# Performance work log

Hardware: AMD Instinct MI355X
Metric: run time of the kernel (lower is better)

## Reference

```python
import jax, jax.numpy as jnp
import numpy as np

B, N, CQ, H, CH = 1, 256, 128, 4, 32  # batch, n_res, c_q(=c_k=c_v), heads, per-head dim


def setup_inputs() -> dict:
    key = jax.random.key(0)
    ks = jax.random.split(key, 12)
    s = 0.02
    q_x = jax.random.normal(ks[0], (B, N, N, CQ), jnp.float32)
    kv_x = jax.random.normal(ks[1], (B, N, N, CQ), jnp.float32)
    # mask bias: 0 where kept, -1e9 where masked (additive mask)
    keep = jax.random.uniform(ks[2], (B, N, 1, 1, N)) < 0.9
    mask_bias = jnp.where(keep, 0.0, -1e9).astype(jnp.float32)
    triangle_bias = jax.random.normal(ks[3], (B, 1, H, N, N), jnp.float32)
    # projection weights, stored per-head as [H, CH, C_in]
    wq = jax.random.normal(ks[4], (H, CH, CQ), jnp.float32) * s
    wk = jax.random.normal(ks[5], (H, CH, CQ), jnp.float32) * s
    wv = jax.random.normal(ks[6], (H, CH, CQ), jnp.float32) * s
    wg = jax.random.normal(ks[7], (H, CH, CQ), jnp.float32) * s
    bg = jax.random.normal(ks[8], (H, CH), jnp.float32) * s + 1.0  # gating bias init 1
    wo = jax.random.normal(ks[9], (CQ, H * CH), jnp.float32) * s
    bo = jnp.zeros((CQ,), jnp.float32)
    return {"q_x": q_x, "kv_x": kv_x, "mask_bias": mask_bias,
            "triangle_bias": triangle_bias, "wq": wq, "wk": wk, "wv": wv,
            "wg": wg, "bg": bg, "wo": wo, "bo": bo}


def reference(q_x, kv_x, mask_bias, triangle_bias, wq, wk, wv, wg, bg, wo, bo):
    scale = 1.0 / np.sqrt(CH).astype(np.float32)
    # project + split heads: [B,N,Q,C] x [H,D,C] -> [B,N,H,Q,D]
    q = jnp.einsum('bnqc,hdc->bnhqd', q_x, wq) * scale
    k = jnp.einsum('bnkc,hdc->bnhkd', kv_x, wk)
    v = jnp.einsum('bnkc,hdc->bnhkd', kv_x, wv)
    # scores + additive biases (mask_bias broadcasts over h,q; triangle over n)
    a = jnp.einsum('bnhqd,bnhkd->bnhqk', q, k) + mask_bias + triangle_bias
    a = jax.nn.softmax(a, axis=-1)
    o = jnp.einsum('bnhqk,bnhkd->bnhqd', a, v)
    o = jnp.swapaxes(o, -2, -3)  # [B,N,Q,H,D]
    # gating
    g = jax.nn.sigmoid(jnp.einsum('bnqc,hdc->bnqhd', q_x, wg) + bg)
    o = o * g
    o = o.reshape(o.shape[:-2] + (H * CH,))  # [B,N,Q,H*D]
    return jnp.einsum('bnqe,ce->bnqc', o, wo) + bo
```

## Files before the change

kernel.cpp:

```cpp
#include <hip/hip_runtime.h>

#define NRES 256
#define CIN  128
#define NH   4
#define DH   32

typedef __attribute__((ext_vector_type(4))) float f32x4;
typedef __attribute__((ext_vector_type(8))) short bf16x8;
typedef unsigned short u16;

#define U_WQG 0
#define U_WKV 32768
#define U_WWO 65536
#define U_QB  131072
#define U_KB  (U_QB + 8388608)
#define U_VT  (U_KB + 8388608)
#define U_GB  (U_VT + 8388608)
#define WS_NEED ((size_t)(U_GB + 8388608) * 2)

__device__ __forceinline__ unsigned pkbf(float a, float b) {
    unsigned ua = __builtin_bit_cast(unsigned, a);
    unsigned ub = __builtin_bit_cast(unsigned, b);
    ua += 0x7fffu + ((ua >> 16) & 1u);
    ub += 0x7fffu + ((ub >> 16) & 1u);
    return __builtin_amdgcn_perm(ub, ua, 0x07060302);
}
__device__ __forceinline__ u16 f2bfu(float f) {
    unsigned u = __builtin_bit_cast(unsigned, f);
    return (u16)((u + 0x7fffu + ((u >> 16) & 1u)) >> 16);
}
__device__ __forceinline__ float bf2f(u16 v) {
    unsigned u = ((unsigned)v) << 16;
    return __builtin_bit_cast(float, u);
}
union bfr { unsigned u[4]; bf16x8 v; };
__device__ __forceinline__ bf16x8 ldcvt8(const float* __restrict__ p) {
    f32x4 a = *(const f32x4*)p; f32x4 b = *(const f32x4*)(p + 4);
    bfr r;
    r.u[0] = pkbf(a[0], a[1]); r.u[1] = pkbf(a[2], a[3]);
    r.u[2] = pkbf(b[0], b[1]); r.u[3] = pkbf(b[2], b[3]);
    return r.v;
}
__device__ __forceinline__ bf16x8 ldcvt8s(const float* __restrict__ p, float sc) {
    f32x4 a = *(const f32x4*)p; f32x4 b = *(const f32x4*)(p + 4);
    bfr r;
    r.u[0] = pkbf(a[0] * sc, a[1] * sc); r.u[1] = pkbf(a[2] * sc, a[3] * sc);
    r.u[2] = pkbf(b[0] * sc, b[1] * sc); r.u[3] = pkbf(b[2] * sc, b[3] * sc);
    return r.v;
}
#define MFMA(a, b, c) __builtin_amdgcn_mfma_f32_16x16x32_bf16((a), (b), (c), 0, 0, 0)

__global__ void wconv(const float* __restrict__ wq, const float* __restrict__ wk,
                      const float* __restrict__ wv, const float* __restrict__ wg,
                      const float* __restrict__ wo, u16* __restrict__ ws)
{
    const int i0 = (blockIdx.x * 256 + threadIdx.x) * 8;
    const float qsc = 0.17677669529663687f;
    const float* src; u16* dst; float sc = 1.f;
    if (i0 < 32768) {
        const int e = i0 >> 7, c = i0 & 127;
        src = (e < 128 ? wq + e * CIN : wg + (e - 128) * CIN) + c;
        if (e < 128) sc = qsc;
        dst = ws + U_WQG + i0;
    } else if (i0 < 65536) {
        const int j = i0 - 32768, e = j >> 7, c = j & 127;
        src = (e < 128 ? wk + e * CIN : wv + (e - 128) * CIN) + c;
        dst = ws + U_WKV + j;
    } else {
        const int j = i0 - 65536;
        src = wo + j; dst = ws + U_WWO + j;
    }
    *(bf16x8*)dst = ldcvt8s(src, sc);
}

__global__ __launch_bounds__(256, 4) void proj(
    const float* __restrict__ q_x, const float* __restrict__ kv_x,
    const float* __restrict__ bg, u16* __restrict__ ws)
{
    const int t = threadIdx.x, lane = t & 63, w = t >> 6;
    const int mrow = lane & 15, grp = lane >> 4;
    const int koff = grp * 8, rbase = grp * 4;
    const int R0 = blockIdx.x * 64;
    const int e0 = w * 64;
    const int ysel = blockIdx.y;
    const float* __restrict__ src = ysel ? kv_x : q_x;
    const u16* __restrict__ W = ws + (ysel ? U_WKV : U_WQG);
    const bool vpath = (ysel == 1) && (w >= 2);

    const f32x4 zf = {0.f, 0.f, 0.f, 0.f};
    f32x4 acc[4][4];
    #pragma unroll
    for (int mt = 0; mt < 4; ++mt)
        #pragma unroll
        for (int nt = 0; nt < 4; ++nt) acc[mt][nt] = zf;

    if (!vpath) {
        #pragma unroll 1
        for (int ct = 0; ct < 4; ++ct) {
            const int c0 = ct * 32 + koff;
            const bf16x8 bw0 = *(const bf16x8*)(W + (e0 +  0 + mrow) * CIN + c0);
            const bf16x8 bw1 = *(const bf16x8*)(W + (e0 + 16 + mrow) * CIN + c0);
            const bf16x8 bw2 = *(const bf16x8*)(W + (e0 + 32 + mrow) * CIN + c0);
            const bf16x8 bw3 = *(const bf16x8*)(W + (e0 + 48 + mrow) * CIN + c0);
            #pragma unroll
            for (int mt = 0; mt < 4; ++mt) {
                const bf16x8 aX = ldcvt8(src + (size_t)(R0 + mt * 16 + mrow) * CIN + c0);
                acc[mt][0] = MFMA(bw0, aX, acc[mt][0]);
                acc[mt][1] = MFMA(bw1, aX, acc[mt][1]);
                acc[mt][2] = MFMA(bw2, aX, acc[mt][2]);
                acc[mt][3] = MFMA(bw3, aX, acc[mt][3]);
            }
        }
    } else {
        #pragma unroll 1
        for (int ct = 0; ct < 4; ++ct) {
            const int c0 = ct * 32 + koff;
            const bf16x8 bw0 = *(const bf16x8*)(W + (e0 +  0 + mrow) * CIN + c0);
            const bf16x8 bw1 = *(const bf16x8*)(W + (e0 + 16 + mrow) * CIN + c0);
            const bf16x8 bw2 = *(const bf16x8*)(W + (e0 + 32 + mrow) * CIN + c0);
            const bf16x8 bw3 = *(const bf16x8*)(W + (e0 + 48 + mrow) * CIN + c0);
            #pragma unroll
            for (int mt = 0; mt < 4; ++mt) {
                const bf16x8 aX = ldcvt8(src + (size_t)(R0 + mt * 16 + mrow) * CIN + c0);
                acc[mt][0] = MFMA(aX, bw0, acc[mt][0]);
                acc[mt][1] = MFMA(aX, bw1, acc[mt][1]);
                acc[mt][2] = MFMA(aX, bw2, acc[mt][2]);
                acc[mt][3] = MFMA(aX, bw3, acc[mt][3]);
            }
        }
    }

    if (!ysel) {
        if (w < 2) {
            #pragma unroll
            for (int mt = 0; mt < 4; ++mt) {
                const size_t row = (size_t)(R0 + mt * 16 + mrow);
                #pragma unroll
                for (int nt = 0; nt < 4; ++nt) {
                    uint2 v;
                    v.x = pkbf(acc[mt][nt][0], acc[mt][nt][1]);
                    v.y = pkbf(acc[mt][nt][2], acc[mt][nt][3]);
                    *(uint2*)&ws[U_QB + row * CIN + e0 + nt * 16 + rbase] = v;
                }
            }
        } else {
            #pragma unroll
            for (int mt = 0; mt < 4; ++mt) {
                const size_t row = (size_t)(R0 + mt * 16 + mrow);
                #pragma unroll
                for (int nt = 0; nt < 4; ++nt) {
                    const int eb = (e0 - 128) + nt * 16 + rbase;
                    const f32x4 bgv = *(const f32x4*)(bg + eb);
                    float g[4];
                    #pragma unroll
                    for (int r = 0; r < 4; ++r)
                        g[r] = 1.f / (1.f + __expf(-(acc[mt][nt][r] + bgv[r])));
                    uint2 v;
                    v.x = pkbf(g[0], g[1]);
                    v.y = pkbf(g[2], g[3]);
                    *(uint2*)&ws[U_GB + row * CIN + eb] = v;
                }
            }
        }
    } else {
        if (w < 2) {
            #pragma unroll
            for (int mt = 0; mt < 4; ++mt) {
                const size_t row = (size_t)(R0 + mt * 16 + mrow);
                #pragma unroll
                for (int nt = 0; nt < 4; ++nt) {
                    uint2 v;
                    v.x = pkbf(acc[mt][nt][0], acc[mt][nt][1]);
                    v.y = pkbf(acc[mt][nt][2], acc[mt][nt][3]);
                    *(uint2*)&ws[U_KB + row * CIN + e0 + nt * 16 + rbase] = v;
                }
            }
        } else {
            const int n = R0 >> 8;
            #pragma unroll
            for (int mt = 0; mt < 4; ++mt) {
                const int k0 = (R0 & 255) + mt * 16 + rbase;
                #pragma unroll
                for (int nt = 0; nt < 4; ++nt) {
                    const int d = (e0 - 128) + nt * 16 + mrow;
                    uint2 v;
                    v.x = pkbf(acc[mt][nt][0], acc[mt][nt][1]);
                    v.y = pkbf(acc[mt][nt][2], acc[mt][nt][3]);
                    *(uint2*)&ws[U_VT + ((size_t)n * 128 + d) * 256 + k0] = v;
                }
            }
        }
    }
}

#define PST 40
__global__ __launch_bounds__(256, 4) void flash(
    const u16* __restrict__ ws, const float* __restrict__ mask_bias,
    const float* __restrict__ tri_bias, float* __restrict__ o_out)
{
    const int h = blockIdx.x, n = blockIdx.y;
    const int t = threadIdx.x, lane = t & 63, w = t >> 6;
    const int mrow = lane & 15, grp = lane >> 4;
    const int koff = grp * 8, rbase = grp * 4;
    const int q0 = w * 64;

    __shared__ u16 Pt[4 * 64 * PST];
    __shared__ float msk[NRES];

    if (t < 64) *(float4*)&msk[t * 4] = *(const float4*)(mask_bias + n * NRES + t * 4);

    const u16* __restrict__ Qb = ws + U_QB + (size_t)n * NRES * CIN;
    const u16* __restrict__ Kb = ws + U_KB + (size_t)n * NRES * CIN;
    const u16* __restrict__ Vt = ws + U_VT + (size_t)n * 128 * 256;
    const u16* __restrict__ Gb = ws + U_GB + (size_t)n * NRES * CIN;
    const float* __restrict__ trih = tri_bias + (size_t)h * NRES * NRES;

    bf16x8 aq[4];
    #pragma unroll
    for (int qt = 0; qt < 4; ++qt)
        aq[qt] = *(const bf16x8*)(Qb + (size_t)(q0 + qt * 16 + mrow) * CIN + h * DH + koff);
    __syncthreads();

    const f32x4 zf = {0.f, 0.f, 0.f, 0.f};
    f32x4 oa[4][2], ls4[4];
    #pragma unroll
    for (int qt = 0; qt < 4; ++qt) { oa[qt][0] = zf; oa[qt][1] = zf; ls4[qt] = zf; }

    u16* __restrict__ pw = &Pt[w * 64 * PST];

    for (int kt = 0; kt < 8; ++kt) {
        const int kb = kt * 32;
        bf16x8 bk0 = *(const bf16x8*)(Kb + (size_t)(kb + mrow) * CIN + h * DH + koff);
        bf16x8 bk1 = *(const bf16x8*)(Kb + (size_t)(kb + 16 + mrow) * CIN + h * DH + koff);
        bf16x8 bv0 = *(const bf16x8*)(Vt + (size_t)(h * DH + mrow) * NRES + kb + koff);
        bf16x8 bv1 = *(const bf16x8*)(Vt + (size_t)(h * DH + 16 + mrow) * NRES + kb + koff);
        const float mb0 = msk[kb + mrow] - 8.f;
        const float mb1 = msk[kb + 16 + mrow] - 8.f;

        #pragma unroll
        for (int h2 = 0; h2 < 2; ++h2) {
            float tr0[2][4], tr1[2][4];
            #pragma unroll
            for (int j = 0; j < 2; ++j) {
                const int qt = h2 * 2 + j;
                const float* __restrict__ trow =
                    trih + (q0 + qt * 16 + rbase) * NRES + kb + mrow;
                #pragma unroll
                for (int r = 0; r < 4; ++r) {
                    tr0[j][r] = trow[r * NRES];
                    tr1[j][r] = trow[r * NRES + 16];
                }
            }
            #pragma unroll
            for (int j = 0; j < 2; ++j) {
                const int qt = h2 * 2 + j;
                f32x4 s0 = MFMA(aq[qt], bk0, zf);
                f32x4 s1 = MFMA(aq[qt], bk1, zf);
                #pragma unroll
                for (int r = 0; r < 4; ++r) {
                    s0[r] = __expf(s0[r] + tr0[j][r] + mb0);
                    s1[r] = __expf(s1[r] + tr1[j][r] + mb1);
                }
                ls4[qt] += s0 + s1;
                #pragma unroll
                for (int r = 0; r < 4; ++r) {
                    pw[(qt * 16 + rbase + r) * PST + mrow]      = f2bfu(s0[r]);
                    pw[(qt * 16 + rbase + r) * PST + 16 + mrow] = f2bfu(s1[r]);
                }
            }
        }
        asm volatile("s_waitcnt lgkmcnt(0)" ::: "memory");
        #pragma unroll
        for (int qt = 0; qt < 4; ++qt) {
            bf16x8 pa = *(const bf16x8*)&pw[(qt * 16 + mrow) * PST + koff];
            oa[qt][0] = MFMA(pa, bv0, oa[qt][0]);
            oa[qt][1] = MFMA(pa, bv1, oa[qt][1]);
        }
    }

    float* __restrict__ orow = o_out + (size_t)n * NRES * CIN + h * DH;
    #pragma unroll
    for (int qt = 0; qt < 4; ++qt) {
        f32x4 lv = ls4[qt];
        #pragma unroll
        for (int xm = 1; xm < 16; xm <<= 1) {
            lv[0] += __shfl_xor(lv[0], xm, 64);
            lv[1] += __shfl_xor(lv[1], xm, 64);
            lv[2] += __shfl_xor(lv[2], xm, 64);
            lv[3] += __shfl_xor(lv[3], xm, 64);
        }
        #pragma unroll
        for (int r = 0; r < 4; ++r) {
            const float inv = 1.f / lv[r];
            const int q = q0 + qt * 16 + rbase + r;
            const float g0 = bf2f(Gb[(size_t)q * CIN + h * DH + mrow]);
            const float g1 = bf2f(Gb[(size_t)q * CIN + h * DH + 16 + mrow]);
            orow[q * CIN + mrow]      = oa[qt][0][r] * inv * g0;
            orow[q * CIN + 16 + mrow] = oa[qt][1][r] * inv * g1;
        }
    }
}

__global__ __launch_bounds__(256, 4) void gout(
    const u16* __restrict__ ws, const float* __restrict__ bo, float* io)
{
    const int t = threadIdx.x, lane = t & 63, w = t >> 6;
    const int mrow = lane & 15, grp = lane >> 4;
    const int koff = grp * 8, rbase = grp * 4;
    const int r0 = blockIdx.x * 128 + w * 32;
    const u16* __restrict__ Wo = ws + U_WWO;

    const f32x4 zf = {0.f, 0.f, 0.f, 0.f};
    f32x4 acc[2][8];
    #pragma unroll
    for (int at = 0; at < 2; ++at)
        #pragma unroll
        for (int nt = 0; nt < 8; ++nt) acc[at][nt] = zf;

    #pragma unroll
    for (int ks = 0; ks < 4; ++ks) {
        const int e0 = ks * 32 + koff;
        bf16x8 a0 = ldcvt8(io + (size_t)(r0 + mrow) * CIN + e0);
        bf16x8 a1 = ldcvt8(io + (size_t)(r0 + 16 + mrow) * CIN + e0);
        #pragma unroll
        for (int nt = 0; nt < 8; ++nt) {
            bf16x8 bw = *(const bf16x8*)(Wo + (nt * 16 + mrow) * CIN + e0);
            acc[0][nt] = MFMA(a0, bw, acc[0][nt]);
            acc[1][nt] = MFMA(a1, bw, acc[1][nt]);
        }
    }

    #pragma unroll
    for (int nt = 0; nt < 8; ++nt) {
        const float bc = bo[nt * 16 + mrow];
        #pragma unroll
        for (int at = 0; at < 2; ++at)
            #pragma unroll
            for (int r = 0; r < 4; ++r)
                io[(size_t)(r0 + at * 16 + rbase + r) * CIN + nt * 16 + mrow] =
                    acc[at][nt][r] + bc;
    }
}

#define KST 32
#define VST 264
#define GST 136

__global__ __launch_bounds__(256, 3) void attn_fb(
    const float* __restrict__ q_x, const float* __restrict__ kv_x,
    const float* __restrict__ mask_bias, const float* __restrict__ tri_bias,
    const float* __restrict__ wq, const float* __restrict__ wk,
    const float* __restrict__ wv, float* __restrict__ o_out)
{
    const int h = blockIdx.x, n = blockIdx.y;
    const int t = threadIdx.x;
    const int lane = t & 63, w = t >> 6;
    const int mrow = lane & 15;
    const int grp  = lane >> 4;
    const int koff = grp * 8;
    const int rbase = grp * 4;
    const int q0 = w * 64;

    __shared__ u16 Ks[NRES * KST];
    __shared__ u16 Vt[DH * VST];
    __shared__ u16 Ptb[4 * 32 * PST];
    __shared__ float msk[NRES];

    if (t < 64) *(float4*)&msk[t * 4] = *(const float4*)(mask_bias + n * NRES + t * 4);

    const float* __restrict__ qxn = q_x  + (size_t)n * NRES * CIN;
    const float* __restrict__ kxn = kv_x + (size_t)n * NRES * CIN;
    const float* __restrict__ wqh = wq + h * DH * CIN;
    const float* __restrict__ wkh = wk + h * DH * CIN;
    const float* __restrict__ wvh = wv + h * DH * CIN;

    f32x4 aq_[4][2], ak_[4][2], av_[4][2];
    const f32x4 zf = {0.f, 0.f, 0.f, 0.f};
    #pragma unroll
    for (int qt = 0; qt < 4; ++qt)
        #pragma unroll
        for (int dt = 0; dt < 2; ++dt) { aq_[qt][dt] = zf; ak_[qt][dt] = zf; av_[qt][dt] = zf; }

    const float qsc = 0.17677669529663687f;
    #pragma unroll
    for (int ct = 0; ct < 4; ++ct) {
        const int c0 = ct * 32 + koff;
        bf16x8 bq0 = ldcvt8s(wqh + mrow * CIN + c0, qsc);
        bf16x8 bq1 = ldcvt8s(wqh + (16 + mrow) * CIN + c0, qsc);
        bf16x8 bk0 = ldcvt8(wkh + mrow * CIN + c0);
        bf16x8 bk1 = ldcvt8(wkh + (16 + mrow) * CIN + c0);
        bf16x8 bv0 = ldcvt8(wvh + mrow * CIN + c0);
        bf16x8 bv1 = ldcvt8(wvh + (16 + mrow) * CIN + c0);
        #pragma unroll
        for (int qt = 0; qt < 4; ++qt) {
            bf16x8 aX = ldcvt8(qxn + (q0 + qt * 16 + mrow) * CIN + c0);
            aq_[qt][0] = MFMA(aX, bq0, aq_[qt][0]);
            aq_[qt][1] = MFMA(aX, bq1, aq_[qt][1]);
            bf16x8 aK = ldcvt8(kxn + (q0 + qt * 16 + mrow) * CIN + c0);
            ak_[qt][0] = MFMA(aK, bk0, ak_[qt][0]);
            ak_[qt][1] = MFMA(aK, bk1, ak_[qt][1]);
            av_[qt][0] = MFMA(aK, bv0, av_[qt][0]);
            av_[qt][1] = MFMA(aK, bv1, av_[qt][1]);
        }
    }

    #pragma unroll
    for (int qt = 0; qt < 4; ++qt)
        #pragma unroll
        for (int dt = 0; dt < 2; ++dt)
            #pragma unroll
            for (int r = 0; r < 4; ++r) {
                const int row = q0 + qt * 16 + rbase + r;
                const int d = dt * 16 + mrow;
                Ks[row * KST + d] = f2bfu(ak_[qt][dt][r]);
                Vt[d * VST + row] = f2bfu(av_[qt][dt][r]);
            }

    u16* __restrict__ pw = &Ptb[w * 32 * PST];
    bf16x8 aq[4];
    #pragma unroll
    for (int h2 = 0; h2 < 2; ++h2) {
        #pragma unroll
        for (int j = 0; j < 2; ++j) {
            const int qt = h2 * 2 + j;
            #pragma unroll
            for (int dt = 0; dt < 2; ++dt)
                #pragma unroll
                for (int r = 0; r < 4; ++r)
                    pw[(j * 16 + rbase + r) * PST + dt * 16 + mrow] = f2bfu(aq_[qt][dt][r]);
        }
        asm volatile("s_waitcnt lgkmcnt(0)" ::: "memory");
        #pragma unroll
        for (int j = 0; j < 2; ++j)
            aq[h2 * 2 + j] = *(const bf16x8*)&pw[(j * 16 + mrow) * PST + koff];
        asm volatile("s_waitcnt lgkmcnt(0)" ::: "memory");
    }
    __syncthreads();

    f32x4 oa[4][2], ls4[4];
    #pragma unroll
    for (int qt = 0; qt < 4; ++qt) { oa[qt][0] = zf; oa[qt][1] = zf; ls4[qt] = zf; }

    const float* __restrict__ trih = tri_bias + (size_t)h * NRES * NRES;

    for (int kt = 0; kt < 8; ++kt) {
        const int kb = kt * 32;
        bf16x8 bk0 = *(const bf16x8*)&Ks[(kb + mrow) * KST + koff];
        bf16x8 bk1 = *(const bf16x8*)&Ks[(kb + 16 + mrow) * KST + koff];
        bf16x8 bv0 = *(const bf16x8*)&Vt[mrow * VST + kb + koff];
        bf16x8 bv1 = *(const bf16x8*)&Vt[(16 + mrow) * VST + kb + koff];
        const float mb0 = msk[kb + mrow] - 8.f;
        const float mb1 = msk[kb + 16 + mrow] - 8.f;

        #pragma unroll
        for (int h2 = 0; h2 < 2; ++h2) {
            float tr0[2][4], tr1[2][4];
            #pragma unroll
            for (int j = 0; j < 2; ++j) {
                const int qt = h2 * 2 + j;
                const float* __restrict__ trow =
                    trih + (q0 + qt * 16 + rbase) * NRES + kb + mrow;
                #pragma unroll
                for (int r = 0; r < 4; ++r) {
                    tr0[j][r] = trow[r * NRES];
                    tr1[j][r] = trow[r * NRES + 16];
                }
            }
            #pragma unroll
            for (int j = 0; j < 2; ++j) {
                const int qt = h2 * 2 + j;
                f32x4 s0 = MFMA(aq[qt], bk0, zf);
                f32x4 s1 = MFMA(aq[qt], bk1, zf);
                #pragma unroll
                for (int r = 0; r < 4; ++r) {
                    s0[r] = __expf(s0[r] + tr0[j][r] + mb0);
                    s1[r] = __expf(s1[r] + tr1[j][r] + mb1);
                }
                ls4[qt] += s0 + s1;
                #pragma unroll
                for (int r = 0; r < 4; ++r) {
                    pw[(j * 16 + rbase + r) * PST + mrow]      = f2bfu(s0[r]);
                    pw[(j * 16 + rbase + r) * PST + 16 + mrow] = f2bfu(s1[r]);
                }
            }
            asm volatile("s_waitcnt lgkmcnt(0)" ::: "memory");
            #pragma unroll
            for (int j = 0; j < 2; ++j) {
                const int qt = h2 * 2 + j;
                bf16x8 pa = *(const bf16x8*)&pw[(j * 16 + mrow) * PST + koff];
                oa[qt][0] = MFMA(pa, bv0, oa[qt][0]);
                oa[qt][1] = MFMA(pa, bv1, oa[qt][1]);
            }
        }
    }

    float* __restrict__ orow = o_out + (size_t)n * NRES * CIN + h * DH;
    #pragma unroll
    for (int qt = 0; qt < 4; ++qt) {
        f32x4 lv = ls4[qt];
        #pragma unroll
        for (int xm = 1; xm < 16; xm <<= 1) {
            lv[0] += __shfl_xor(lv[0], xm, 64);
            lv[1] += __shfl_xor(lv[1], xm, 64);
            lv[2] += __shfl_xor(lv[2], xm, 64);
            lv[3] += __shfl_xor(lv[3], xm, 64);
        }
        #pragma unroll
        for (int r = 0; r < 4; ++r) {
            const float inv = 1.f / lv[r];
            const int q = q0 + qt * 16 + rbase + r;
            orow[q * CIN + mrow]      = oa[qt][0][r] * inv;
            orow[q * CIN + 16 + mrow] = oa[qt][1][r] * inv;
        }
    }
}

__global__ __launch_bounds__(256, 4) void gate_fb(
    const float* __restrict__ q_x, const float* __restrict__ wg,
    const float* __restrict__ bg, const float* __restrict__ wo,
    const float* __restrict__ bo, float* io)
{
    const int t = threadIdx.x;
    const int lane = t & 63, w = t >> 6;
    const int mrow = lane & 15, grp = lane >> 4;
    const int koff = grp * 8, rbase = grp * 4;
    const int r0 = blockIdx.x * 128 + w * 32;

    __shared__ u16 Gt[4 * 32 * GST];
    u16* __restrict__ gw = &Gt[w * 32 * GST];

    const f32x4 zf = {0.f, 0.f, 0.f, 0.f};
    f32x4 acc[2][8];
    #pragma unroll
    for (int at = 0; at < 2; ++at)
        #pragma unroll
        for (int nt = 0; nt < 8; ++nt) acc[at][nt] = zf;

    #pragma unroll
    for (int ks = 0; ks < 4; ++ks) {
        const int c0 = ks * 32 + koff;
        bf16x8 ax0 = ldcvt8(q_x + (size_t)(r0 + mrow) * CIN + c0);
        bf16x8 ax1 = ldcvt8(q_x + (size_t)(r0 + 16 + mrow) * CIN + c0);
        #pragma unroll
        for (int nt = 0; nt < 8; ++nt) {
            bf16x8 bw = ldcvt8(wg + (nt * 16 + mrow) * CIN + c0);
            acc[0][nt] = MFMA(ax0, bw, acc[0][nt]);
            acc[1][nt] = MFMA(ax1, bw, acc[1][nt]);
        }
    }

    #pragma unroll
    for (int nt = 0; nt < 8; ++nt) {
        const float bge = bg[nt * 16 + mrow];
        #pragma unroll
        for (int at = 0; at < 2; ++at)
            #pragma unroll
            for (int r = 0; r < 4; ++r) {
                const int qg = r0 + at * 16 + rbase + r;
                const float ov = io[(size_t)qg * CIN + nt * 16 + mrow];
                const float g = 1.f / (1.f + __expf(-(acc[at][nt][r] + bge)));
                gw[(at * 16 + rbase + r) * GST + nt * 16 + mrow] = f2bfu(ov * g);
            }
    }
    asm volatile("s_waitcnt lgkmcnt(0)" ::: "memory");

    f32x4 acc2[2][8];
    #pragma unroll
    for (int at = 0; at < 2; ++at)
        #pragma unroll
        for (int nt = 0; nt < 8; ++nt) acc2[at][nt] = zf;

    #pragma unroll
    for (int ks = 0; ks < 4; ++ks) {
        const int e0 = ks * 32 + koff;
        bf16x8 ag0 = *(const bf16x8*)&gw[mrow * GST + e0];
        bf16x8 ag1 = *(const bf16x8*)&gw[(16 + mrow) * GST + e0];
        #pragma unroll
        for (int nt = 0; nt < 8; ++nt) {
            bf16x8 bw = ldcvt8(wo + (nt * 16 + mrow) * CIN + e0);
            acc2[0][nt] = MFMA(ag0, bw, acc2[0][nt]);
            acc2[1][nt] = MFMA(ag1, bw, acc2[1][nt]);
        }
    }

    #pragma unroll
    for (int nt = 0; nt < 8; ++nt) {
        const float boc = bo[nt * 16 + mrow];
        #pragma unroll
        for (int at = 0; at < 2; ++at)
            #pragma unroll
            for (int r = 0; r < 4; ++r)
                io[(size_t)(r0 + at * 16 + rbase + r) * CIN + nt * 16 + mrow] =
                    acc2[at][nt][r] + boc;
    }
}

extern "C" void kernel_launch(void* const* d_in, const int* in_sizes, int n_in,
                              void* d_out, int out_size, void* d_ws, size_t ws_size,
                              hipStream_t stream) {
    const float* q_x  = (const float*)d_in[0];
    const float* kv_x = (const float*)d_in[1];
    const float* mask = (const float*)d_in[2];
    const float* tri  = (const float*)d_in[3];
    const float* wq   = (const float*)d_in[4];
    const float* wk   = (const float*)d_in[5];
    const float* wv   = (const float*)d_in[6];
    const float* wg   = (const float*)d_in[7];
    const float* bg   = (const float*)d_in[8];
    const float* wo   = (const float*)d_in[9];
    const float* bo   = (const float*)d_in[10];
    float* out = (float*)d_out;

    if (ws_size >= WS_NEED) {
        u16* ws16 = (u16*)d_ws;
        wconv<<<40, 256, 0, stream>>>(wq, wk, wv, wg, wo, ws16);
        proj<<<dim3(1024, 2), 256, 0, stream>>>(q_x, kv_x, bg, ws16);
        flash<<<dim3(NH, NRES), 256, 0, stream>>>(ws16, mask, tri, out);
        gout<<<512, 256, 0, stream>>>(ws16, bo, out);
    } else {
        attn_fb<<<dim3(NH, NRES), 256, 0, stream>>>(q_x, kv_x, mask, tri, wq, wk, wv, out);
        gate_fb<<<(NRES * NRES) / 128, 256, 0, stream>>>(q_x, wg, bg, wo, bo, out);
    }
}
```

Measured before the change: 232.7 us.

## Fuse projection, attention and output GEMM into one per-row kernel

Replaces the separate proj, flash and gout launches with a single kernel that runs one block per residue row n. Each block first computes the Q/G/K/V projections for its 256 rows, then loops over the four heads doing the attention, and writes the gated output as bf16 into the Q buffer in place. It then runs the output projection from that buffer and adds the bias. This removes two kernel launches and the fp32 round trip of the intermediate attention output through global memory. In exchange the grid drops to 256 blocks of 4 waves each, which is far less parallelism and latency hiding than the earlier grids, and the per-head work inside a block runs serially.

```diff
diff --git a/kernel.cpp b/kernel.cpp
--- a/kernel.cpp
+++ b/kernel.cpp
@@ -73,272 +73,270 @@
     *(bf16x8*)dst = ldcvt8s(src, sc);
 }
 
-__global__ __launch_bounds__(256, 4) void proj(
+#define PST 40
+__global__ __launch_bounds__(256) void fused(
     const float* __restrict__ q_x, const float* __restrict__ kv_x,
-    const float* __restrict__ bg, u16* __restrict__ ws)
+    const float* __restrict__ bg, const float* __restrict__ mask_bias,
+    const float* __restrict__ tri_bias, const float* __restrict__ bo,
+    u16* __restrict__ ws, float* __restrict__ out)
 {
+    const int n = blockIdx.x;
     const int t = threadIdx.x, lane = t & 63, w = t >> 6;
     const int mrow = lane & 15, grp = lane >> 4;
     const int koff = grp * 8, rbase = grp * 4;
-    const int R0 = blockIdx.x * 64;
-    const int e0 = w * 64;
-    const int ysel = blockIdx.y;
-    const float* __restrict__ src = ysel ? kv_x : q_x;
-    const u16* __restrict__ W = ws + (ysel ? U_WKV : U_WQG);
-    const bool vpath = (ysel == 1) && (w >= 2);
-
-    const f32x4 zf = {0.f, 0.f, 0.f, 0.f};
-    f32x4 acc[4][4];
-    #pragma unroll
-    for (int mt = 0; mt < 4; ++mt)
-        #pragma unroll
-        for (int nt = 0; nt < 4; ++nt) acc[mt][nt] = zf;
-
-    if (!vpath) {
-        #pragma unroll 1
-        for (int ct = 0; ct < 4; ++ct) {
-            const int c0 = ct * 32 + koff;
-            const bf16x8 bw0 = *(const bf16x8*)(W + (e0 +  0 + mrow) * CIN + c0);
-            const bf16x8 bw1 = *(const bf16x8*)(W + (e0 + 16 + mrow) * CIN + c0);
-            const bf16x8 bw2 = *(const bf16x8*)(W + (e0 + 32 + mrow) * CIN + c0);
-            const bf16x8 bw3 = *(const bf16x8*)(W + (e0 + 48 + mrow) * CIN + c0);
-            #pragma unroll
-            for (int mt = 0; mt < 4; ++mt) {
-                const bf16x8 aX = ldcvt8(src + (size_t)(R0 + mt * 16 + mrow) * CIN + c0);
-                acc[mt][0] = MFMA(bw0, aX, acc[mt][0]);
-                acc[mt][1] = MFMA(bw1, aX, acc[mt][1]);
-                acc[mt][2] = MFMA(bw2, aX, acc[mt][2]);
-                acc[mt][3] = MFMA(bw3, aX, acc[mt][3]);
-            }
-        }
-    } else {
-        #pragma unroll 1
-        for (int ct = 0; ct < 4; ++ct) {
-            const int c0 = ct * 32 + koff;
-            const bf16x8 bw0 = *(const bf16x8*)(W + (e0 +  0 + mrow) * CIN + c0);
-            const bf16x8 bw1 = *(const bf16x8*)(W + (e0 + 16 + mrow) * CIN + c0);
-            const bf16x8 bw2 = *(const bf16x8*)(W + (e0 + 32 + mrow) * CIN + c0);
-            const bf16x8 bw3 = *(const bf16x8*)(W + (e0 + 48 + mrow) * CIN + c0);
-            #pragma unroll
-            for (int mt = 0; mt < 4; ++mt) {
-                const bf16x8 aX = ldcvt8(src + (size_t)(R0 + mt * 16 + mrow) * CIN + c0);
-                acc[mt][0] = MFMA(aX, bw0, acc[mt][0]);
-                acc[mt][1] = MFMA(aX, bw1, acc[mt][1]);
-                acc[mt][2] = MFMA(aX, bw2, acc[mt][2]);
-                acc[mt][3] = MFMA(aX, bw3, acc[mt][3]);
-            }
-        }
-    }
-
-    if (!ysel) {
-        if (w < 2) {
-            #pragma unroll
-            for (int mt = 0; mt < 4; ++mt) {
-                const size_t row = (size_t)(R0 + mt * 16 + mrow);
-                #pragma unroll
-                for (int nt = 0; nt < 4; ++nt) {
-                    uint2 v;
-                    v.x = pkbf(acc[mt][nt][0], acc[mt][nt][1]);
-                    v.y = pkbf(acc[mt][nt][2], acc[mt][nt][3]);
-                    *(uint2*)&ws[U_QB + row * CIN + e0 + nt * 16 + rbase] = v;
-                }
-            }
-        } else {
-            #pragma unroll
-            for (int mt = 0; mt < 4; ++mt) {
-                const size_t row = (size_t)(R0 + mt * 16 + mrow);
-                #pragma unroll
-                for (int nt = 0; nt < 4; ++nt) {
-                    const int eb = (e0 - 128) + nt * 16 + rbase;
-                    const f32x4 bgv = *(const f32x4*)(bg + eb);
-                    float g[4];
-                    #pragma unroll
-                    for (int r = 0; r < 4; ++r)
-                        g[r] = 1.f / (1.f + __expf(-(acc[mt][nt][r] + bgv[r])));
-                    uint2 v;
-                    v.x = pkbf(g[0], g[1]);
-                    v.y = pkbf(g[2], g[3]);
-                    *(uint2*)&ws[U_GB + row * CIN + eb] = v;
-                }
-            }
-        }
-    } else {
-        if (w < 2) {
-            #pragma unroll
-            for (int mt = 0; mt < 4; ++mt) {
-                const size_t row = (size_t)(R0 + mt * 16 + mrow);
-                #pragma unroll
-                for (int nt = 0; nt < 4; ++nt) {
-                    uint2 v;
-                    v.x = pkbf(acc[mt][nt][0], acc[mt][nt][1]);
-                    v.y = pkbf(acc[mt][nt][2], acc[mt][nt][3]);
-                    *(uint2*)&ws[U_KB + row * CIN + e0 + nt * 16 + rbase] = v;
-                }
-            }
-        } else {
-            const int n = R0 >> 8;
-            #pragma unroll
-            for (int mt = 0; mt < 4; ++mt) {
-                const int k0 = (R0 & 255) + mt * 16 + rbase;
-                #pragma unroll
-                for (int nt = 0; nt < 4; ++nt) {
-                    const int d = (e0 - 128) + nt * 16 + mrow;
-                    uint2 v;
-                    v.x = pkbf(acc[mt][nt][0], acc[mt][nt][1]);
-                    v.y = pkbf(acc[mt][nt][2], acc[mt][nt][3]);
-                    *(uint2*)&ws[U_VT + ((size_t)n * 128 + d) * 256 + k0] = v;
-                }
-            }
-        }
-    }
-}
-
-#define PST 40
-__global__ __launch_bounds__(256, 4) void flash(
-    const u16* __restrict__ ws, const float* __restrict__ mask_bias,
-    const float* __restrict__ tri_bias, float* __restrict__ o_out)
-{
-    const int h = blockIdx.x, n = blockIdx.y;
-    const int t = threadIdx.x, lane = t & 63, w = t >> 6;
-    const int mrow = lane & 15, grp = lane >> 4;
-    const int koff = grp * 8, rbase = grp * 4;
-    const int q0 = w * 64;
 
     __shared__ u16 Pt[4 * 64 * PST];
     __shared__ float msk[NRES];
 
     if (t < 64) *(float4*)&msk[t * 4] = *(const float4*)(mask_bias + n * NRES + t * 4);
 
-    const u16* __restrict__ Qb = ws + U_QB + (size_t)n * NRES * CIN;
+    #pragma unroll 1
+    for (int u = 0; u < 8; ++u) {
+        const int tid  = u * 4 + w;
+        const int ysel = tid & 1;
+        const int rb   = (tid >> 1) & 3;
+        const int e0   = ((tid >> 3) & 3) * 64;
+        const int R0   = n * 256 + rb * 64;
+        const float* __restrict__ src = ysel ? kv_x : q_x;
+        const u16* __restrict__ W = ws + (ysel ? U_WKV : U_WQG);
+        const bool vpath = ysel && (e0 >= 128);
+
+        const f32x4 zf = {0.f, 0.f, 0.f, 0.f};
+        f32x4 acc[4][4];
+        #pragma unroll
+        for (int mt = 0; mt < 4; ++mt)
+            #pragma unroll
+            for (int nt = 0; nt < 4; ++nt) acc[mt][nt] = zf;
+
+        if (!vpath) {
+            #pragma unroll 2
+            for (int ct = 0; ct < 4; ++ct) {
+                const int c0 = ct * 32 + koff;
+                const bf16x8 bw0 = *(const bf16x8*)(W + (e0 +  0 + mrow) * CIN + c0);
+                const bf16x8 bw1 = *(const bf16x8*)(W + (e0 + 16 + mrow) * CIN + c0);
+                const bf16x8 bw2 = *(const bf16x8*)(W + (e0 + 32 + mrow) * CIN + c0);
+                const bf16x8 bw3 = *(const bf16x8*)(W + (e0 + 48 + mrow) * CIN + c0);
+                #pragma unroll
+                for (int mt = 0; mt < 4; ++mt) {
+                    const bf16x8 aX = ldcvt8(src + (size_t)(R0 + mt * 16 + mrow) * CIN + c0);
+                    acc[mt][0] = MFMA(bw0, aX, acc[mt][0]);
+                    acc[mt][1] = MFMA(bw1, aX, acc[mt][1]);
+                    acc[mt][2] = MFMA(bw2, aX, acc[mt][2]);
+                    acc[mt][3] = MFMA(bw3, aX, acc[mt][3]);
+                }
+            }
+        } else {
+            #pragma unroll 2
+            for (int ct = 0; ct < 4; ++ct) {
+                const int c0 = ct * 32 + koff;
+                const bf16x8 bw0 = *(const bf16x8*)(W + (e0 +  0 + mrow) * CIN + c0);
+                const bf16x8 bw1 = *(const bf16x8*)(W + (e0 + 16 + mrow) * CIN + c0);
+                const bf16x8 bw2 = *(const bf16x8*)(W + (e0 + 32 + mrow) * CIN + c0);
+                const bf16x8 bw3 = *(const bf16x8*)(W + (e0 + 48 + mrow) * CIN + c0);
+                #pragma unroll
+                for (int mt = 0; mt < 4; ++mt) {
+                    const bf16x8 aX = ldcvt8(src + (size_t)(R0 + mt * 16 + mrow) * CIN + c0);
+                    acc[mt][0] = MFMA(aX, bw0, acc[mt][0]);
+                    acc[mt][1] = MFMA(aX, bw1, acc[mt][1]);
+                    acc[mt][2] = MFMA(aX, bw2, acc[mt][2]);
+                    acc[mt][3] = MFMA(aX, bw3, acc[mt][3]);
+                }
+            }
+        }
+
+        if (!ysel) {
+            if (e0 < 128) {
+                #pragma unroll
+                for (int mt = 0; mt < 4; ++mt) {
+                    const size_t row = (size_t)(R0 + mt * 16 + mrow);
+                    #pragma unroll
+                    for (int nt = 0; nt < 4; ++nt) {
+                        uint2 v;
+                        v.x = pkbf(acc[mt][nt][0], acc[mt][nt][1]);
+                        v.y = pkbf(acc[mt][nt][2], acc[mt][nt][3]);
+                        *(uint2*)&ws[U_QB + row * CIN + e0 + nt * 16 + rbase] = v;
+                    }
+                }
+            } else {
+                #pragma unroll
+                for (int mt = 0; mt < 4; ++mt) {
+                    const size_t row = (size_t)(R0 + mt * 16 + mrow);
+                    #pragma unroll
+                    for (int nt = 0; nt < 4; ++nt) {
+                        const int eb = (e0 - 128) + nt * 16 + rbase;
+                        const f32x4 bgv = *(const f32x4*)(bg + eb);
+                        float g[4];
+                        #pragma unroll
+                        for (int r = 0; r < 4; ++r)
+                            g[r] = 1.f / (1.f + __expf(-(acc[mt][nt][r] + bgv[r])));
+                        uint2 v;
+                        v.x = pkbf(g[0], g[1]);
+                        v.y = pkbf(g[2], g[3]);
+                        *(uint2*)&ws[U_GB + row * CIN + eb] = v;
+                    }
+                }
+            }
+        } else {
+            if (e0 < 128) {
+                #pragma unroll
+                for (int mt = 0; mt < 4; ++mt) {
+                    const size_t row = (size_t)(R0 + mt * 16 + mrow);
+                    #pragma unroll
+                    for (int nt = 0; nt < 4; ++nt) {
+                        uint2 v;
+                        v.x = pkbf(acc[mt][nt][0], acc[mt][nt][1]);
+                        v.y = pkbf(acc[mt][nt][2], acc[mt][nt][3]);
+                        *(uint2*)&ws[U_KB + row * CIN + e0 + nt * 16 + rbase] = v;
+                    }
+                }
+            } else {
+                #pragma unroll
+                for (int mt = 0; mt < 4; ++mt) {
+                    const int k0 = rb * 64 + mt * 16 + rbase;
+                    #pragma unroll
+                    for (int nt = 0; nt < 4; ++nt) {
+                        const int d = (e0 - 128) + nt * 16 + mrow;
+                        uint2 v;
+                        v.x = pkbf(acc[mt][nt][0], acc[mt][nt][1]);
+                        v.y = pkbf(acc[mt][nt][2], acc[mt][nt][3]);
+                        *(uint2*)&ws[U_VT + ((size_t)n * 128 + d) * 256 + k0] = v;
+                    }
+                }
+            }
+        }
+    }
+
+    __syncthreads();
+
+    u16* __restrict__ QOg = ws + U_QB + (size_t)n * NRES * CIN;
     const u16* __restrict__ Kb = ws + U_KB + (size_t)n * NRES * CIN;
     const u16* __restrict__ Vt = ws + U_VT + (size_t)n * 128 * 256;
     const u16* __restrict__ Gb = ws + U_GB + (size_t)n * NRES * CIN;
-    const float* __restrict__ trih = tri_bias + (size_t)h * NRES * NRES;
-
-    bf16x8 aq[4];
-    #pragma unroll
-    for (int qt = 0; qt < 4; ++qt)
-        aq[qt] = *(const bf16x8*)(Qb + (size_t)(q0 + qt * 16 + mrow) * CIN + h * DH + koff);
-    __syncthreads();
-
+    const int q0 = w * 64;
     const f32x4 zf = {0.f, 0.f, 0.f, 0.f};
-    f32x4 oa[4][2], ls4[4];
-    #pragma unroll
-    for (int qt = 0; qt < 4; ++qt) { oa[qt][0] = zf; oa[qt][1] = zf; ls4[qt] = zf; }
-
     u16* __restrict__ pw = &Pt[w * 64 * PST];
 
-    for (int kt = 0; kt < 8; ++kt) {
-        const int kb = kt * 32;
-        bf16x8 bk0 = *(const bf16x8*)(Kb + (size_t)(kb + mrow) * CIN + h * DH + koff);
-        bf16x8 bk1 = *(const bf16x8*)(Kb + (size_t)(kb + 16 + mrow) * CIN + h * DH + koff);
-        bf16x8 bv0 = *(const bf16x8*)(Vt + (size_t)(h * DH + mrow) * NRES + kb + koff);
-        bf16x8 bv1 = *(const bf16x8*)(Vt + (size_t)(h * DH + 16 + mrow) * NRES + kb + koff);
-        const float mb0 = msk[kb + mrow] - 8.f;
-        const float mb1 = msk[kb + 16 + mrow] - 8.f;
-
-        #pragma unroll
-        for (int h2 = 0; h2 < 2; ++h2) {
-            float tr0[2][4], tr1[2][4];
-            #pragma unroll
-            for (int j = 0; j < 2; ++j) {
-                const int qt = h2 * 2 + j;
-                const float* __restrict__ trow =
-                    trih + (q0 + qt * 16 + rbase) * NRES + kb + mrow;
-                #pragma unroll
-                for (int r = 0; r < 4; ++r) {
-                    tr0[j][r] = trow[r * NRES];
-                    tr1[j][r] = trow[r * NRES + 16];
-                }
-            }
-            #pragma unroll
-            for (int j = 0; j < 2; ++j) {
-                const int qt = h2 * 2 + j;
-                f32x4 s0 = MFMA(aq[qt], bk0, zf);
-                f32x4 s1 = MFMA(aq[qt], bk1, zf);
-                #pragma unroll
-                for (int r = 0; r < 4; ++r) {
-                    s0[r] = __expf(s0[r] + tr0[j][r] + mb0);
-                    s1[r] = __expf(s1[r] + tr1[j][r] + mb1);
-                }
-                ls4[qt] += s0 + s1;
-                #pragma unroll
-                for (int r = 0; r < 4; ++r) {
-                    pw[(qt * 16 + rbase + r) * PST + mrow]      = f2bfu(s0[r]);
-                    pw[(qt * 16 + rbase + r) * PST + 16 + mrow] = f2bfu(s1[r]);
-                }
-            }
-        }
-        asm volatile("s_waitcnt lgkmcnt(0)" ::: "memory");
+    #pragma unroll 1
+    for (int h = 0; h < 4; ++h) {
+        bf16x8 aqh[4];
+        #pragma unroll
+        for (int qt = 0; qt < 4; ++qt)
+            aqh[qt] = *(const bf16x8*)(QOg + (size_t)(q0 + qt * 16 + mrow) * CIN + h * DH + koff);
+
+        f32x4 oa[4][2], ls4[4];
+        #pragma unroll
+        for (int qt = 0; qt < 4; ++qt) { oa[qt][0] = zf; oa[qt][1] = zf; ls4[qt] = zf; }
+
+        const float* __restrict__ trih = tri_bias + (size_t)h * NRES * NRES;
+
+        for (int kt = 0; kt < 8; ++kt) {
+            const int kb = kt * 32;
+            bf16x8 bk0 = *(const bf16x8*)(Kb + (size_t)(kb + mrow) * CIN + h * DH + koff);
+            bf16x8 bk1 = *(const bf16x8*)(Kb + (size_t)(kb + 16 + mrow) * CIN + h * DH + koff);
+            bf16x8 bv0 = *(const bf16x8*)(Vt + (size_t)(h * DH + mrow) * NRES + kb + koff);
+            bf16x8 bv1 = *(const bf16x8*)(Vt + (size_t)(h * DH + 16 + mrow) * NRES + kb + koff);
+            const float mb0 = msk[kb + mrow] - 8.f;
+            const float mb1 = msk[kb + 16 + mrow] - 8.f;
+
+            #pragma unroll
+            for (int h2 = 0; h2 < 2; ++h2) {
+                float tr0[2][4], tr1[2][4];
+                #pragma unroll
+                for (int j = 0; j < 2; ++j) {
+                    const int qt = h2 * 2 + j;
+                    const float* __restrict__ trow =
+                        trih + (q0 + qt * 16 + rbase) * NRES + kb + mrow;
+                    #pragma unroll
+                    for (int r = 0; r < 4; ++r) {
+                        tr0[j][r] = trow[r * NRES];
+                        tr1[j][r] = trow[r * NRES + 16];
+                    }
+                }
+                #pragma unroll
+                for (int j = 0; j < 2; ++j) {
+                    const int qt = h2 * 2 + j;
+                    f32x4 s0 = MFMA(aqh[qt], bk0, zf);
+                    f32x4 s1 = MFMA(aqh[qt], bk1, zf);
+                    #pragma unroll
+                    for (int r = 0; r < 4; ++r) {
+                        s0[r] = __expf(s0[r] + tr0[j][r] + mb0);
+                        s1[r] = __expf(s1[r] + tr1[j][r] + mb1);
+                    }
+                    ls4[qt] += s0 + s1;
+                    #pragma unroll
+                    for (int r = 0; r < 4; ++r) {
+                        pw[(qt * 16 + rbase + r) * PST + mrow]      = f2bfu(s0[r]);
+                        pw[(qt * 16 + rbase + r) * PST + 16 + mrow] = f2bfu(s1[r]);
+                    }
+                }
+            }
+            asm volatile("s_waitcnt lgkmcnt(0)" ::: "memory");
+            #pragma unroll
+            for (int qt = 0; qt < 4; ++qt) {
+                bf16x8 pa = *(const bf16x8*)&pw[(qt * 16 + mrow) * PST + koff];
+                oa[qt][0] = MFMA(pa, bv0, oa[qt][0]);
+                oa[qt][1] = MFMA(pa, bv1, oa[qt][1]);
+            }
+        }
+
         #pragma unroll
         for (int qt = 0; qt < 4; ++qt) {
-            bf16x8 pa = *(const bf16x8*)&pw[(qt * 16 + mrow) * PST + koff];
-            oa[qt][0] = MFMA(pa, bv0, oa[qt][0]);
-            oa[qt][1] = MFMA(pa, bv1, oa[qt][1]);
-        }
-    }
-
-    float* __restrict__ orow = o_out + (size_t)n * NRES * CIN + h * DH;
-    #pragma unroll
-    for (int qt = 0; qt < 4; ++qt) {
-        f32x4 lv = ls4[qt];
-        #pragma unroll
-        for (int xm = 1; xm < 16; xm <<= 1) {
-            lv[0] += __shfl_xor(lv[0], xm, 64);
-            lv[1] += __shfl_xor(lv[1], xm, 64);
-            lv[2] += __shfl_xor(lv[2], xm, 64);
-            lv[3] += __shfl_xor(lv[3], xm, 64);
-        }
-        #pragma unroll
-        for (int r = 0; r < 4; ++r) {
-            const float inv = 1.f / lv[r];
-            const int q = q0 + qt * 16 + rbase + r;
-            const float g0 = bf2f(Gb[(size_t)q * CIN + h * DH + mrow]);
-            const float g1 = bf2f(Gb[(size_t)q * CIN + h * DH + 16 + mrow]);
-            orow[q * CIN + mrow]      = oa[qt][0][r] * inv * g0;
-            orow[q * CIN + 16 + mrow] = oa[qt][1][r] * inv * g1;
-        }
-    }
-}
-
-__global__ __launch_bounds__(256, 4) void gout(
-    const u16* __restrict__ ws, const float* __restrict__ bo, float* io)
-{
-    const int t = threadIdx.x, lane = t & 63, w = t >> 6;
-    const int mrow = lane & 15, grp = lane >> 4;
-    const int koff = grp * 8, rbase = grp * 4;
-    const int r0 = blockIdx.x * 128 + w * 32;
+            f32x4 lv = ls4[qt];
+            #pragma unroll
+            for (int xm = 1; xm < 16; xm <<= 1) {
+                lv[0] += __shfl_xor(lv[0], xm, 64);
+                lv[1] += __shfl_xor(lv[1], xm, 64);
+                lv[2] += __shfl_xor(lv[2], xm, 64);
+                lv[3] += __shfl_xor(lv[3], xm, 64);
+            }
+            #pragma unroll
+            for (int r = 0; r < 4; ++r) {
+                const float inv = 1.f / lv[r];
+                const int q = q0 + qt * 16 + rbase + r;
+                const float g0 = bf2f(Gb[(size_t)q * CIN + h * DH + mrow]);
+                const float g1 = bf2f(Gb[(size_t)q * CIN + h * DH + 16 + mrow]);
+                QOg[(size_t)q * CIN + h * DH + mrow]      = f2bfu(oa[qt][0][r] * inv * g0);
+                QOg[(size_t)q * CIN + h * DH + 16 + mrow] = f2bfu(oa[qt][1][r] * inv * g1);
+            }
+        }
+    }
+
+    asm volatile("s_waitcnt vmcnt(0)" ::: "memory");
+
     const u16* __restrict__ Wo = ws + U_WWO;
-
-    const f32x4 zf = {0.f, 0.f, 0.f, 0.f};
-    f32x4 acc[2][8];
-    #pragma unroll
-    for (int at = 0; at < 2; ++at)
-        #pragma unroll
-        for (int nt = 0; nt < 8; ++nt) acc[at][nt] = zf;
-
-    #pragma unroll
-    for (int ks = 0; ks < 4; ++ks) {
-        const int e0 = ks * 32 + koff;
-        bf16x8 a0 = ldcvt8(io + (size_t)(r0 + mrow) * CIN + e0);
-        bf16x8 a1 = ldcvt8(io + (size_t)(r0 + 16 + mrow) * CIN + e0);
+    float* __restrict__ outn = out + (size_t)n * NRES * CIN;
+    #pragma unroll 1
+    for (int sb = 0; sb < 2; ++sb) {
+        const int r0s = q0 + sb * 32;
+        f32x4 acc2[2][8];
+        #pragma unroll
+        for (int at = 0; at < 2; ++at)
+            #pragma unroll
+            for (int nt = 0; nt < 8; ++nt) acc2[at][nt] = zf;
+
+        #pragma unroll
+        for (int ks = 0; ks < 4; ++ks) {
+            const int e0k = ks * 32 + koff;
+            const bf16x8 a0 = *(const bf16x8*)(QOg + (size_t)(r0s + mrow) * CIN + e0k);
+            const bf16x8 a1 = *(const bf16x8*)(QOg + (size_t)(r0s + 16 + mrow) * CIN + e0k);
+            #pragma unroll
+            for (int nt = 0; nt < 8; ++nt) {
+                const bf16x8 bw = *(const bf16x8*)(Wo + (nt * 16 + mrow) * CIN + e0k);
+                acc2[0][nt] = MFMA(a0, bw, acc2[0][nt]);
+                acc2[1][nt] = MFMA(a1, bw, acc2[1][nt]);
+            }
+        }
+
         #pragma unroll
         for (int nt = 0; nt < 8; ++nt) {
-            bf16x8 bw = *(const bf16x8*)(Wo + (nt * 16 + mrow) * CIN + e0);
-            acc[0][nt] = MFMA(a0, bw, acc[0][nt]);
-            acc[1][nt] = MFMA(a1, bw, acc[1][nt]);
-        }
-    }
-
-    #pragma unroll
-    for (int nt = 0; nt < 8; ++nt) {
-        const float bc = bo[nt * 16 + mrow];
-        #pragma unroll
-        for (int at = 0; at < 2; ++at)
-            #pragma unroll
-            for (int r = 0; r < 4; ++r)
-                io[(size_t)(r0 + at * 16 + rbase + r) * CIN + nt * 16 + mrow] =
-                    acc[at][nt][r] + bc;
+            const float bc = bo[nt * 16 + mrow];
+            #pragma unroll
+            for (int at = 0; at < 2; ++at)
+                #pragma unroll
+                for (int r = 0; r < 4; ++r)
+                    outn[(size_t)(r0s + at * 16 + rbase + r) * CIN + nt * 16 + mrow] =
+                        acc2[at][nt][r] + bc;
+        }
     }
 }
 
@@ -614,9 +612,7 @@
     if (ws_size >= WS_NEED) {
         u16* ws16 = (u16*)d_ws;
         wconv<<<40, 256, 0, stream>>>(wq, wk, wv, wg, wo, ws16);
-        proj<<<dim3(1024, 2), 256, 0, stream>>>(q_x, kv_x, bg, ws16);
-        flash<<<dim3(NH, NRES), 256, 0, stream>>>(ws16, mask, tri, out);
-        gout<<<512, 256, 0, stream>>>(ws16, bo, out);
+        fused<<<NRES, 256, 0, stream>>>(q_x, kv_x, bg, mask, tri, bo, ws16, out);
     } else {
         attn_fb<<<dim3(NH, NRES), 256, 0, stream>>>(q_x, kv_x, mask, tri, wq, wk, wv, out);
         gate_fb<<<(NRES * NRES) / 128, 256, 0, stream>>>(q_x, wg, bg, wo, bo, out);
```

Measured after the change: 271.6 us. +16.7%, slower.

## Transpose MFMA operands for vectorized bias loads and keep gated output in bf16

Applied to the files above, without the earlier changes.

The flash kernel swaps the MFMA A/B operands so that each lane holds four consecutive key columns. This lets the triangle bias and mask load as float4 vectors, P be written to LDS as packed uint2, and the row-sum reduction shrink to two shuffles. The gated attention output is written as bf16 over the Q buffer in the workspace instead of as fp32 to the output. gout then reads it directly without conversion and writes float4 vectors. The intent is to cut global traffic and scattered scalar accesses, at the cost of an extra bf16 rounding on the intermediate.

```diff
diff --git a/kernel.cpp b/kernel.cpp
--- a/kernel.cpp
+++ b/kernel.cpp
@@ -195,8 +195,8 @@
 
 #define PST 40
 __global__ __launch_bounds__(256, 4) void flash(
-    const u16* __restrict__ ws, const float* __restrict__ mask_bias,
-    const float* __restrict__ tri_bias, float* __restrict__ o_out)
+    u16* __restrict__ ws, const float* __restrict__ mask_bias,
+    const float* __restrict__ tri_bias)
 {
     const int h = blockIdx.x, n = blockIdx.y;
     const int t = threadIdx.x, lane = t & 63, w = t >> 6;
@@ -209,7 +209,7 @@
 
     if (t < 64) *(float4*)&msk[t * 4] = *(const float4*)(mask_bias + n * NRES + t * 4);
 
-    const u16* __restrict__ Qb = ws + U_QB + (size_t)n * NRES * CIN;
+    u16* __restrict__ QOg = ws + U_QB + (size_t)n * NRES * CIN;
     const u16* __restrict__ Kb = ws + U_KB + (size_t)n * NRES * CIN;
     const u16* __restrict__ Vt = ws + U_VT + (size_t)n * 128 * 256;
     const u16* __restrict__ Gb = ws + U_GB + (size_t)n * NRES * CIN;
@@ -218,13 +218,14 @@
     bf16x8 aq[4];
     #pragma unroll
     for (int qt = 0; qt < 4; ++qt)
-        aq[qt] = *(const bf16x8*)(Qb + (size_t)(q0 + qt * 16 + mrow) * CIN + h * DH + koff);
+        aq[qt] = *(const bf16x8*)(QOg + (size_t)(q0 + qt * 16 + mrow) * CIN + h * DH + koff);
     __syncthreads();
 
     const f32x4 zf = {0.f, 0.f, 0.f, 0.f};
-    f32x4 oa[4][2], ls4[4];
-    #pragma unroll
-    for (int qt = 0; qt < 4; ++qt) { oa[qt][0] = zf; oa[qt][1] = zf; ls4[qt] = zf; }
+    f32x4 oa[4][2];
+    float ls[4];
+    #pragma unroll
+    for (int qt = 0; qt < 4; ++qt) { oa[qt][0] = zf; oa[qt][1] = zf; ls[qt] = 0.f; }
 
     u16* __restrict__ pw = &Pt[w * 64 * PST];
 
@@ -234,81 +235,71 @@
         bf16x8 bk1 = *(const bf16x8*)(Kb + (size_t)(kb + 16 + mrow) * CIN + h * DH + koff);
         bf16x8 bv0 = *(const bf16x8*)(Vt + (size_t)(h * DH + mrow) * NRES + kb + koff);
         bf16x8 bv1 = *(const bf16x8*)(Vt + (size_t)(h * DH + 16 + mrow) * NRES + kb + koff);
-        const float mb0 = msk[kb + mrow] - 8.f;
-        const float mb1 = msk[kb + 16 + mrow] - 8.f;
-
-        #pragma unroll
-        for (int h2 = 0; h2 < 2; ++h2) {
-            float tr0[2][4], tr1[2][4];
-            #pragma unroll
-            for (int j = 0; j < 2; ++j) {
-                const int qt = h2 * 2 + j;
-                const float* __restrict__ trow =
-                    trih + (q0 + qt * 16 + rbase) * NRES + kb + mrow;
-                #pragma unroll
-                for (int r = 0; r < 4; ++r) {
-                    tr0[j][r] = trow[r * NRES];
-                    tr1[j][r] = trow[r * NRES + 16];
-                }
-            }
-            #pragma unroll
-            for (int j = 0; j < 2; ++j) {
-                const int qt = h2 * 2 + j;
-                f32x4 s0 = MFMA(aq[qt], bk0, zf);
-                f32x4 s1 = MFMA(aq[qt], bk1, zf);
-                #pragma unroll
-                for (int r = 0; r < 4; ++r) {
-                    s0[r] = __expf(s0[r] + tr0[j][r] + mb0);
-                    s1[r] = __expf(s1[r] + tr1[j][r] + mb1);
-                }
-                ls4[qt] += s0 + s1;
-                #pragma unroll
-                for (int r = 0; r < 4; ++r) {
-                    pw[(qt * 16 + rbase + r) * PST + mrow]      = f2bfu(s0[r]);
-                    pw[(qt * 16 + rbase + r) * PST + 16 + mrow] = f2bfu(s1[r]);
-                }
-            }
+        const f32x4 m0 = *(const f32x4*)&msk[kb + rbase];
+        const f32x4 m1 = *(const f32x4*)&msk[kb + 16 + rbase];
+
+        #pragma unroll
+        for (int qt = 0; qt < 4; ++qt) {
+            const int q = q0 + qt * 16 + mrow;
+            const f32x4 t0 = *(const f32x4*)(trih + (size_t)q * NRES + kb + rbase);
+            const f32x4 t1 = *(const f32x4*)(trih + (size_t)q * NRES + kb + 16 + rbase);
+            f32x4 s0 = MFMA(bk0, aq[qt], zf);
+            f32x4 s1 = MFMA(bk1, aq[qt], zf);
+            float part = 0.f;
+            #pragma unroll
+            for (int r = 0; r < 4; ++r) {
+                s0[r] = __expf(s0[r] + t0[r] + m0[r] - 8.f);
+                s1[r] = __expf(s1[r] + t1[r] + m1[r] - 8.f);
+                part += s0[r] + s1[r];
+            }
+            ls[qt] += part;
+            uint2 v0, v1;
+            v0.x = pkbf(s0[0], s0[1]); v0.y = pkbf(s0[2], s0[3]);
+            v1.x = pkbf(s1[0], s1[1]); v1.y = pkbf(s1[2], s1[3]);
+            *(uint2*)&pw[(qt * 16 + mrow) * PST + rbase]      = v0;
+            *(uint2*)&pw[(qt * 16 + mrow) * PST + 16 + rbase] = v1;
         }
         asm volatile("s_waitcnt lgkmcnt(0)" ::: "memory");
+        __builtin_amdgcn_sched_barrier(0);
         #pragma unroll
         for (int qt = 0; qt < 4; ++qt) {
             bf16x8 pa = *(const bf16x8*)&pw[(qt * 16 + mrow) * PST + koff];
-            oa[qt][0] = MFMA(pa, bv0, oa[qt][0]);
-            oa[qt][1] = MFMA(pa, bv1, oa[qt][1]);
-        }
-    }
-
-    float* __restrict__ orow = o_out + (size_t)n * NRES * CIN + h * DH;
+            oa[qt][0] = MFMA(bv0, pa, oa[qt][0]);
+            oa[qt][1] = MFMA(bv1, pa, oa[qt][1]);
+        }
+    }
+
     #pragma unroll
     for (int qt = 0; qt < 4; ++qt) {
-        f32x4 lv = ls4[qt];
-        #pragma unroll
-        for (int xm = 1; xm < 16; xm <<= 1) {
-            lv[0] += __shfl_xor(lv[0], xm, 64);
-            lv[1] += __shfl_xor(lv[1], xm, 64);
-            lv[2] += __shfl_xor(lv[2], xm, 64);
-            lv[3] += __shfl_xor(lv[3], xm, 64);
-        }
-        #pragma unroll
-        for (int r = 0; r < 4; ++r) {
-            const float inv = 1.f / lv[r];
-            const int q = q0 + qt * 16 + rbase + r;
-            const float g0 = bf2f(Gb[(size_t)q * CIN + h * DH + mrow]);
-            const float g1 = bf2f(Gb[(size_t)q * CIN + h * DH + 16 + mrow]);
-            orow[q * CIN + mrow]      = oa[qt][0][r] * inv * g0;
-            orow[q * CIN + 16 + mrow] = oa[qt][1][r] * inv * g1;
+        float lv = ls[qt];
+        lv += __shfl_xor(lv, 16, 64);
+        lv += __shfl_xor(lv, 32, 64);
+        const float inv = 1.f / lv;
+        const int q = q0 + qt * 16 + mrow;
+        #pragma unroll
+        for (int half = 0; half < 2; ++half) {
+            const size_t off = (size_t)q * CIN + h * DH + half * 16 + rbase;
+            const uint2 gv = *(const uint2*)&Gb[off];
+            const float g0 = bf2f((u16)(gv.x)),        g1 = bf2f((u16)(gv.x >> 16));
+            const float g2 = bf2f((u16)(gv.y)),        g3 = bf2f((u16)(gv.y >> 16));
+            uint2 ov;
+            ov.x = pkbf(oa[qt][half][0] * inv * g0, oa[qt][half][1] * inv * g1);
+            ov.y = pkbf(oa[qt][half][2] * inv * g2, oa[qt][half][3] * inv * g3);
+            *(uint2*)&QOg[off] = ov;
         }
     }
 }
 
 __global__ __launch_bounds__(256, 4) void gout(
-    const u16* __restrict__ ws, const float* __restrict__ bo, float* io)
+    const u16* __restrict__ ws, const float* __restrict__ bo,
+    float* __restrict__ out)
 {
     const int t = threadIdx.x, lane = t & 63, w = t >> 6;
     const int mrow = lane & 15, grp = lane >> 4;
     const int koff = grp * 8, rbase = grp * 4;
     const int r0 = blockIdx.x * 128 + w * 32;
     const u16* __restrict__ Wo = ws + U_WWO;
+    const u16* __restrict__ QOg = ws + U_QB;
 
     const f32x4 zf = {0.f, 0.f, 0.f, 0.f};
     f32x4 acc[2][8];
@@ -320,25 +311,24 @@
     #pragma unroll
     for (int ks = 0; ks < 4; ++ks) {
         const int e0 = ks * 32 + koff;
-        bf16x8 a0 = ldcvt8(io + (size_t)(r0 + mrow) * CIN + e0);
-        bf16x8 a1 = ldcvt8(io + (size_t)(r0 + 16 + mrow) * CIN + e0);
+        const bf16x8 a0 = *(const bf16x8*)(QOg + (size_t)(r0 + mrow) * CIN + e0);
+        const bf16x8 a1 = *(const bf16x8*)(QOg + (size_t)(r0 + 16 + mrow) * CIN + e0);
         #pragma unroll
         for (int nt = 0; nt < 8; ++nt) {
-            bf16x8 bw = *(const bf16x8*)(Wo + (nt * 16 + mrow) * CIN + e0);
-            acc[0][nt] = MFMA(a0, bw, acc[0][nt]);
-            acc[1][nt] = MFMA(a1, bw, acc[1][nt]);
+            const bf16x8 bw = *(const bf16x8*)(Wo + (nt * 16 + mrow) * CIN + e0);
+            acc[0][nt] = MFMA(bw, a0, acc[0][nt]);
+            acc[1][nt] = MFMA(bw, a1, acc[1][nt]);
         }
     }
 
     #pragma unroll
     for (int nt = 0; nt < 8; ++nt) {
-        const float bc = bo[nt * 16 + mrow];
-        #pragma unroll
-        for (int at = 0; at < 2; ++at)
-            #pragma unroll
-            for (int r = 0; r < 4; ++r)
-                io[(size_t)(r0 + at * 16 + rbase + r) * CIN + nt * 16 + mrow] =
-                    acc[at][nt][r] + bc;
+        const f32x4 bov = *(const f32x4*)&bo[nt * 16 + rbase];
+        #pragma unroll
+        for (int at = 0; at < 2; ++at) {
+            const f32x4 v = acc[at][nt] + bov;
+            *(f32x4*)&out[(size_t)(r0 + at * 16 + mrow) * CIN + nt * 16 + rbase] = v;
+        }
     }
 }
 
@@ -615,7 +605,7 @@
         u16* ws16 = (u16*)d_ws;
         wconv<<<40, 256, 0, stream>>>(wq, wk, wv, wg, wo, ws16);
         proj<<<dim3(1024, 2), 256, 0, stream>>>(q_x, kv_x, bg, ws16);
-        flash<<<dim3(NH, NRES), 256, 0, stream>>>(ws16, mask, tri, out);
+        flash<<<dim3(NH, NRES), 256, 0, stream>>>(ws16, mask, tri);
         gout<<<512, 256, 0, stream>>>(ws16, bo, out);
     } else {
         attn_fb<<<dim3(NH, NRES), 256, 0, stream>>>(q_x, kv_x, mask, tri, wq, wk, wv, out);
```

New measurement: 247.1 us. 6.2% more time.
